# Optimization experiments

Measured on AMD Instinct MI355X. Metric: run time of the kernel, lower is better.

Reference implementation:

```python
import jax, jax.numpy as jnp
import numpy as np

N = 100001      # item_num + 1
D = 64          # hidden_units
NNZ = 3200000   # number of nonzeros in encoder_adj (avg degree ~32)


def setup_inputs() -> dict:
    key = jax.random.key(0)
    k1, k2, k3, k4 = jax.random.split(key, 4)
    row_idx = jax.random.randint(k1, (NNZ,), 0, N, dtype=jnp.int32)
    col_idx = jax.random.randint(k2, (NNZ,), 0, N, dtype=jnp.int32)
    adj_vals = jax.random.uniform(k3, (NNZ,), dtype=jnp.float32)
    emb_weight = jax.random.normal(k4, (N, D), dtype=jnp.float32)
    return {"row_idx": row_idx, "col_idx": col_idx, "adj_vals": adj_vals,
            "emb_weight": emb_weight}


def _spmm(row_idx, col_idx, vals, x):
    # COO SpMM: out[r] += vals[e] * x[col[e]]  -> [N, D]
    gathered = vals[:, None] * x[col_idx]          # [NNZ, D]
    return jax.ops.segment_sum(gathered, row_idx, num_segments=N)


def reference(row_idx, col_idx, adj_vals, emb_weight):
    e0 = emb_weight                                 # ego embeddings
    e1 = _spmm(row_idx, col_idx, adj_vals, e0)      # GCN layer 1
    e2 = _spmm(row_idx, col_idx, adj_vals, e1)      # GCN layer 2
    summed = e0 + e1 + e2                           # sum(embeds)
    return (summed, e0, e1, e2)
```

## Files before the change

kernel.cpp:

```cpp
#include <hip/hip_runtime.h>
#include <stdint.h>

#define DHID 64
#define G_BLOCKS 1024
#define BMAX 1024
#define RPB 128
#define CAP 4608

static inline size_t align256(size_t x) { return (x + 255) & ~(size_t)255; }


__global__ void zero_f32(float* __restrict__ p, size_t n) {
  size_t i = (size_t)blockIdx.x * blockDim.x + threadIdx.x;
  if (i < n) p[i] = 0.f;
}


__global__ __launch_bounds__(256) void
a1_hist_k(const int* __restrict__ row, int* __restrict__ histGB,
          int nnz, int B, int chunk) {
  __shared__ int h[BMAX];
  for (int i = threadIdx.x; i < B; i += 256) h[i] = 0;
  __syncthreads();
  int g = blockIdx.x;
  int s = g * chunk, e = min(nnz, s + chunk);
  int j = s + threadIdx.x;
  for (; j + 768 < e; j += 1024) {
    int r0 = row[j], r1 = row[j + 256], r2 = row[j + 512], r3 = row[j + 768];
    atomicAdd(&h[r0 >> 7], 1);
    atomicAdd(&h[r1 >> 7], 1);
    atomicAdd(&h[r2 >> 7], 1);
    atomicAdd(&h[r3 >> 7], 1);
  }
  for (; j < e; j += 256)
    atomicAdd(&h[row[j] >> 7], 1);
  __syncthreads();
  for (int i = threadIdx.x; i < B; i += 256)
    histGB[i * G_BLOCKS + g] = h[i];
}

__global__ __launch_bounds__(256) void
scan_gb_k(const int* __restrict__ histGB, int* __restrict__ offGB,
          int* __restrict__ btot, int B) {
  __shared__ int wsum[4];
  int b = blockIdx.x, t = threadIdx.x, lane = t & 63, w = t >> 6;
  int v[4];
  int s4 = 0;
#pragma unroll
  for (int i = 0; i < 4; ++i) {
    v[i] = histGB[b * G_BLOCKS + t * 4 + i];
    s4 += v[i];
  }
  int incl = s4;
#pragma unroll
  for (int off = 1; off < 64; off <<= 1) {
    int u = __shfl_up(incl, off);
    if (lane >= off) incl += u;
  }
  if (lane == 63) wsum[w] = incl;
  __syncthreads();
  int run = incl - s4;
  for (int w2 = 0; w2 < w; ++w2) run += wsum[w2];
#pragma unroll
  for (int i = 0; i < 4; ++i) {
    offGB[b * G_BLOCKS + t * 4 + i] = run;
    run += v[i];
  }
  if (t == 0) btot[b] = wsum[0] + wsum[1] + wsum[2] + wsum[3];
}

__global__ void scan_b_k(const int* __restrict__ btot, int* __restrict__ base, int B) {
  __shared__ int wsum[4];
  int t = threadIdx.x, lane = t & 63, w = t >> 6;
  int v[8];
  int s = 0;
#pragma unroll
  for (int i = 0; i < 8; ++i) {
    int idx = t * 8 + i;
    v[i] = (idx < B) ? btot[idx] : 0;
    s += v[i];
  }
  int incl = s;
#pragma unroll
  for (int off = 1; off < 64; off <<= 1) {
    int u = __shfl_up(incl, off);
    if (lane >= off) incl += u;
  }
  if (lane == 63) wsum[w] = incl;
  __syncthreads();
  int run = incl - s;
  for (int w2 = 0; w2 < w; ++w2) run += wsum[w2];
#pragma unroll
  for (int i = 0; i < 8; ++i) {
    int idx = t * 8 + i;
    if (idx <= B) base[idx] = run;
    run += v[i];
  }
}

__global__ __launch_bounds__(256) void
a2_scatter_k(const int* __restrict__ row, const int* __restrict__ col,
             const float* __restrict__ val, const int* __restrict__ base,
             const int* __restrict__ offGB, int2* __restrict__ stage,
             int nnz, int B, int chunk) {
  __shared__ int cur[BMAX];
  int g = blockIdx.x;
  for (int i = threadIdx.x; i < B; i += 256)
    cur[i] = base[i] + offGB[i * G_BLOCKS + g];
  __syncthreads();
  int s = g * chunk, e = min(nnz, s + chunk);
  int j = s + threadIdx.x;
  for (; j + 768 < e; j += 1024) {
    int r0 = row[j], r1 = row[j + 256], r2 = row[j + 512], r3 = row[j + 768];
    int c0 = col[j], c1 = col[j + 256], c2 = col[j + 512], c3 = col[j + 768];
    float v0 = val[j], v1 = val[j + 256], v2 = val[j + 512], v3 = val[j + 768];
    int p0 = atomicAdd(&cur[r0 >> 7], 1);
    int p1 = atomicAdd(&cur[r1 >> 7], 1);
    int p2 = atomicAdd(&cur[r2 >> 7], 1);
    int p3 = atomicAdd(&cur[r3 >> 7], 1);
    int2 q0; q0.x = ((r0 & 127) << 24) | c0; q0.y = __float_as_int(v0);
    int2 q1; q1.x = ((r1 & 127) << 24) | c1; q1.y = __float_as_int(v1);
    int2 q2; q2.x = ((r2 & 127) << 24) | c2; q2.y = __float_as_int(v2);
    int2 q3; q3.x = ((r3 & 127) << 24) | c3; q3.y = __float_as_int(v3);
    stage[p0] = q0;
    stage[p1] = q1;
    stage[p2] = q2;
    stage[p3] = q3;
  }
  for (; j < e; j += 256) {
    int r = row[j];
    int pos = atomicAdd(&cur[r >> 7], 1);
    int2 p;
    p.x = ((r & 127) << 24) | col[j];
    p.y = __float_as_int(val[j]);
    stage[pos] = p;
  }
}


__global__ __launch_bounds__(512) void
spmm_csr_k(const int* __restrict__ base, const int2* __restrict__ stage,
           const float* __restrict__ x, float* __restrict__ y, int n) {
  __shared__ int2 ebuf[CAP];
  __shared__ int h[RPB], rowoff[RPB], cur[RPB];
  __shared__ int w0sum;
  int b = blockIdx.x, t = threadIdx.x;
  int lane = t & 63, w = t >> 6;
  if (t < RPB) h[t] = 0;
  __syncthreads();
  int s = __builtin_amdgcn_readfirstlane(base[b]);
  int e = __builtin_amdgcn_readfirstlane(base[b + 1]);
  int cnt = e - s;
  if (cnt <= CAP) {
    for (int j = s + t; j < e; j += 512)
      atomicAdd(&h[((unsigned)stage[j].x) >> 24], 1);
    __syncthreads();
    int v = 0, part = 0;
    if (t < RPB) {
      v = h[t];
      int incl = v;
#pragma unroll
      for (int off = 1; off < 64; off <<= 1) {
        int u = __shfl_up(incl, off);
        if (lane >= off) incl += u;
      }
      if (t == 63) w0sum = incl;
      part = incl - v;
    }
    __syncthreads();
    if (t < RPB) {
      int excl = part + ((t >= 64) ? w0sum : 0);
      rowoff[t] = excl;
      cur[t] = excl;
    }
    __syncthreads();
    for (int j = s + t; j < e; j += 512) {
      int2 p = stage[j];
      int r = ((unsigned)p.x) >> 24;
      int pos = atomicAdd(&cur[r], 1);
      int2 q; q.x = p.x & 0xFFFFFF; q.y = p.y;
      ebuf[pos] = q;
    }
    __syncthreads();
    for (int rr = w * 16; rr < w * 16 + 16; ++rr) {
      int R = (b << 7) + rr;
      if (R >= n) continue;
      int start = __builtin_amdgcn_readfirstlane(rowoff[rr]);
      int end   = __builtin_amdgcn_readfirstlane(cur[rr]);
      float acc = 0.f;
      int k = start;
      for (; k + 8 <= end; k += 8) {
        int2 e0 = ebuf[k + 0], e1 = ebuf[k + 1], e2 = ebuf[k + 2], e3 = ebuf[k + 3];
        int2 e4 = ebuf[k + 4], e5 = ebuf[k + 5], e6 = ebuf[k + 6], e7 = ebuf[k + 7];
        float x0 = x[((size_t)e0.x << 6) + lane];
        float x1 = x[((size_t)e1.x << 6) + lane];
        float x2 = x[((size_t)e2.x << 6) + lane];
        float x3 = x[((size_t)e3.x << 6) + lane];
        float x4 = x[((size_t)e4.x << 6) + lane];
        float x5 = x[((size_t)e5.x << 6) + lane];
        float x6 = x[((size_t)e6.x << 6) + lane];
        float x7 = x[((size_t)e7.x << 6) + lane];
        acc += __int_as_float(e0.y) * x0;
        acc += __int_as_float(e1.y) * x1;
        acc += __int_as_float(e2.y) * x2;
        acc += __int_as_float(e3.y) * x3;
        acc += __int_as_float(e4.y) * x4;
        acc += __int_as_float(e5.y) * x5;
        acc += __int_as_float(e6.y) * x6;
        acc += __int_as_float(e7.y) * x7;
      }
      for (; k < end; ++k) {
        int2 p = ebuf[k];
        acc += __int_as_float(p.y) * x[((size_t)p.x << 6) + lane];
      }
      y[((size_t)R << 6) + lane] = acc;
    }
  } else {
    for (int rr = w * 16; rr < w * 16 + 16; ++rr) {
      int R = (b << 7) + rr;
      if (R >= n) continue;
      float acc = 0.f;
      for (int j = s; j < e; ++j) {
        int2 p = stage[j];
        if ((int)(((unsigned)p.x) >> 24) == rr)
          acc += __int_as_float(p.y) * x[((size_t)(p.x & 0xFFFFFF) << 6) + lane];
      }
      y[((size_t)R << 6) + lane] = acc;
    }
  }
}

__global__ __launch_bounds__(512) void
spmm_csr_fused_k(const int* __restrict__ base, const int2* __restrict__ stage,
                 const float* __restrict__ e0g, const float* __restrict__ e1g,
                 float* __restrict__ e2g, float* __restrict__ summed,
                 float* __restrict__ e0out, int n) {
  __shared__ int2 ebuf[CAP];
  __shared__ int h[RPB], rowoff[RPB], cur[RPB];
  __shared__ int w0sum;
  int b = blockIdx.x, t = threadIdx.x;
  int lane = t & 63, w = t >> 6;
  if (t < RPB) h[t] = 0;
  __syncthreads();
  int s = __builtin_amdgcn_readfirstlane(base[b]);
  int e = __builtin_amdgcn_readfirstlane(base[b + 1]);
  int cnt = e - s;
  if (cnt <= CAP) {
    for (int j = s + t; j < e; j += 512)
      atomicAdd(&h[((unsigned)stage[j].x) >> 24], 1);
    __syncthreads();
    int v = 0, part = 0;
    if (t < RPB) {
      v = h[t];
      int incl = v;
#pragma unroll
      for (int off = 1; off < 64; off <<= 1) {
        int u = __shfl_up(incl, off);
        if (lane >= off) incl += u;
      }
      if (t == 63) w0sum = incl;
      part = incl - v;
    }
    __syncthreads();
    if (t < RPB) {
      int excl = part + ((t >= 64) ? w0sum : 0);
      rowoff[t] = excl;
      cur[t] = excl;
    }
    __syncthreads();
    for (int j = s + t; j < e; j += 512) {
      int2 p = stage[j];
      int r = ((unsigned)p.x) >> 24;
      int pos = atomicAdd(&cur[r], 1);
      int2 q; q.x = p.x & 0xFFFFFF; q.y = p.y;
      ebuf[pos] = q;
    }
    __syncthreads();
    for (int rr = w * 16; rr < w * 16 + 16; ++rr) {
      int R = (b << 7) + rr;
      if (R >= n) continue;
      int start = __builtin_amdgcn_readfirstlane(rowoff[rr]);
      int end   = __builtin_amdgcn_readfirstlane(cur[rr]);
      float acc = 0.f;
      int k = start;
      for (; k + 8 <= end; k += 8) {
        int2 ea = ebuf[k + 0], eb = ebuf[k + 1], ec = ebuf[k + 2], ed = ebuf[k + 3];
        int2 ee = ebuf[k + 4], ef = ebuf[k + 5], eg = ebuf[k + 6], eh = ebuf[k + 7];
        float x0 = e1g[((size_t)ea.x << 6) + lane];
        float x1 = e1g[((size_t)eb.x << 6) + lane];
        float x2 = e1g[((size_t)ec.x << 6) + lane];
        float x3 = e1g[((size_t)ed.x << 6) + lane];
        float x4 = e1g[((size_t)ee.x << 6) + lane];
        float x5 = e1g[((size_t)ef.x << 6) + lane];
        float x6 = e1g[((size_t)eg.x << 6) + lane];
        float x7 = e1g[((size_t)eh.x << 6) + lane];
        acc += __int_as_float(ea.y) * x0;
        acc += __int_as_float(eb.y) * x1;
        acc += __int_as_float(ec.y) * x2;
        acc += __int_as_float(ed.y) * x3;
        acc += __int_as_float(ee.y) * x4;
        acc += __int_as_float(ef.y) * x5;
        acc += __int_as_float(eg.y) * x6;
        acc += __int_as_float(eh.y) * x7;
      }
      for (; k < end; ++k) {
        int2 p = ebuf[k];
        acc += __int_as_float(p.y) * e1g[((size_t)p.x << 6) + lane];
      }
      size_t o = ((size_t)R << 6) + lane;
      float v0 = e0g[o];
      float v1 = e1g[o];
      e2g[o] = acc;
      summed[o] = v0 + v1 + acc;
      e0out[o] = v0;
    }
  } else {
    for (int rr = w * 16; rr < w * 16 + 16; ++rr) {
      int R = (b << 7) + rr;
      if (R >= n) continue;
      float acc = 0.f;
      for (int j = s; j < e; ++j) {
        int2 p = stage[j];
        if ((int)(((unsigned)p.x) >> 24) == rr)
          acc += __int_as_float(p.y) * e1g[((size_t)(p.x & 0xFFFFFF) << 6) + lane];
      }
      size_t o = ((size_t)R << 6) + lane;
      float v0 = e0g[o];
      float v1 = e1g[o];
      e2g[o] = acc;
      summed[o] = v0 + v1 + acc;
      e0out[o] = v0;
    }
  }
}


__global__ void spmm_atomic_k(const int* __restrict__ row, const int* __restrict__ col,
                              const float* __restrict__ val, const float* __restrict__ x,
                              float* __restrict__ y, int nnz) {
  int wave = (blockIdx.x * blockDim.x + threadIdx.x) >> 6;
  int lane = threadIdx.x & 63;
  if (wave >= nnz) return;
  int r = row[wave]; int c = col[wave]; float v = val[wave];
  atomicAdd(&y[(size_t)r * DHID + lane], v * x[(size_t)c * DHID + lane]);
}

__global__ void sum_k(const float4* __restrict__ e0, const float4* __restrict__ e1,
                      const float4* __restrict__ e2, float4* __restrict__ summed,
                      float4* __restrict__ e0out, int n4) {
  int i = blockIdx.x * blockDim.x + threadIdx.x;
  if (i < n4) {
    float4 a = e0[i], b = e1[i], c = e2[i];
    float4 s;
    s.x = a.x + b.x + c.x;
    s.y = a.y + b.y + c.y;
    s.z = a.z + b.z + c.z;
    s.w = a.w + b.w + c.w;
    summed[i] = s;
    e0out[i] = a;
  }
}

extern "C" void kernel_launch(void* const* d_in, const int* in_sizes, int n_in,
                              void* d_out, int out_size, void* d_ws, size_t ws_size,
                              hipStream_t stream) {
  const int*   row = (const int*)d_in[0];
  const int*   col = (const int*)d_in[1];
  const float* val = (const float*)d_in[2];
  const float* emb = (const float*)d_in[3];
  int nnz = in_sizes[0];
  int n   = in_sizes[3] / DHID;
  size_t ND = (size_t)n * DHID;

  float* out    = (float*)d_out;
  float* summed = out;
  float* e0o    = out + ND;
  float* e1     = out + 2 * ND;
  float* e2     = out + 3 * ND;

  int B  = (n + RPB - 1) / RPB;
  int chunk = (nnz + G_BLOCKS - 1) / G_BLOCKS;

  size_t o0 = 0;
  size_t histGB_off = o0; o0 += align256((size_t)B * G_BLOCKS * 4);
  size_t offGB_off  = o0; o0 += align256((size_t)B * G_BLOCKS * 4);
  size_t btot_off   = o0; o0 += align256((size_t)B * 4);
  size_t base_off   = o0; o0 += align256((size_t)(B + 1) * 4);
  size_t stage_off  = o0; o0 += align256((size_t)nnz * 8);
  size_t need_sorted = o0;

  bool use_sorted = (ws_size >= need_sorted) && (B <= BMAX) && (n < (1 << 24));

  int n4 = (int)(ND / 4);
  int sb = (n4 + 255) / 256;
  int wb = (int)(((size_t)nnz * 64 + 255) / 256);

  if (use_sorted) {
    uint8_t* w = (uint8_t*)d_ws;
    int*  histGB = (int*)(w + histGB_off);
    int*  offGB  = (int*)(w + offGB_off);
    int*  btot   = (int*)(w + btot_off);
    int*  base   = (int*)(w + base_off);
    int2* stage  = (int2*)(w + stage_off);

    a1_hist_k<<<G_BLOCKS, 256, 0, stream>>>(row, histGB, nnz, B, chunk);
    scan_gb_k<<<B, 256, 0, stream>>>(histGB, offGB, btot, B);
    scan_b_k<<<1, 256, 0, stream>>>(btot, base, B);
    a2_scatter_k<<<G_BLOCKS, 256, 0, stream>>>(row, col, val, base, offGB, stage,
                                               nnz, B, chunk);

    spmm_csr_k<<<B, 512, 0, stream>>>(base, stage, emb, e1, n);
    spmm_csr_fused_k<<<B, 512, 0, stream>>>(base, stage, emb, e1, e2, summed, e0o, n);
  } else {
    zero_f32<<<(int)((ND + 255) / 256), 256, 0, stream>>>(e1, ND);
    spmm_atomic_k<<<wb, 256, 0, stream>>>(row, col, val, emb, e1, nnz);
    zero_f32<<<(int)((ND + 255) / 256), 256, 0, stream>>>(e2, ND);
    spmm_atomic_k<<<wb, 256, 0, stream>>>(row, col, val, e1, e2, nnz);
    sum_k<<<sb, 256, 0, stream>>>((const float4*)emb, (const float4*)e1,
                                  (const float4*)e2, (float4*)summed,
                                  (float4*)e0o, n4);
  }
}
```

Measured before the change: 432.6 us.

## Bucket edges by column phase so SpMM gathers sweep column ranges in lockstep

In both SpMM kernels, each block's edges are now bucketed by (column range of 16K rows, local row) rather than by local row alone. The gather loop then walks phase by phase, and all waves keep 16 row accumulators in registers. Within a phase every block reads from the same slice of x at roughly the same time, which is meant to improve L2/MALL hit rates for the random gathers. The cost is a scan over 1024 keys instead of 128, more LDS for the offset arrays, more registers, and a shorter unroll (4 instead of 8) for rows that are now split into smaller segments.

```diff
diff --git a/kernel.cpp b/kernel.cpp
--- a/kernel.cpp
+++ b/kernel.cpp
@@ -6,6 +6,9 @@
 #define BMAX 1024
 #define RPB 128
 #define CAP 4608
+#define PH_SHIFT 14
+#define NPHMAX 8
+#define NKEY (NPHMAX * RPB)
 
 static inline size_t align256(size_t x) { return (x + 255) & ~(size_t)255; }
 
@@ -140,80 +143,81 @@
 
 __global__ __launch_bounds__(512) void
 spmm_csr_k(const int* __restrict__ base, const int2* __restrict__ stage,
-           const float* __restrict__ x, float* __restrict__ y, int n) {
+           const float* __restrict__ x, float* __restrict__ y, int n, int nph) {
   __shared__ int2 ebuf[CAP];
-  __shared__ int h[RPB], rowoff[RPB], cur[RPB];
-  __shared__ int w0sum;
+  __shared__ int rowoff[NKEY], cur[NKEY];
+  __shared__ int wsum[8];
   int b = blockIdx.x, t = threadIdx.x;
   int lane = t & 63, w = t >> 6;
-  if (t < RPB) h[t] = 0;
+  cur[t] = 0; cur[t + 512] = 0;
   __syncthreads();
   int s = __builtin_amdgcn_readfirstlane(base[b]);
   int e = __builtin_amdgcn_readfirstlane(base[b + 1]);
   int cnt = e - s;
   if (cnt <= CAP) {
-    for (int j = s + t; j < e; j += 512)
-      atomicAdd(&h[((unsigned)stage[j].x) >> 24], 1);
-    __syncthreads();
-    int v = 0, part = 0;
-    if (t < RPB) {
-      v = h[t];
-      int incl = v;
-#pragma unroll
-      for (int off = 1; off < 64; off <<= 1) {
-        int u = __shfl_up(incl, off);
-        if (lane >= off) incl += u;
-      }
-      if (t == 63) w0sum = incl;
-      part = incl - v;
-    }
-    __syncthreads();
-    if (t < RPB) {
-      int excl = part + ((t >= 64) ? w0sum : 0);
-      rowoff[t] = excl;
-      cur[t] = excl;
-    }
-    __syncthreads();
     for (int j = s + t; j < e; j += 512) {
       int2 p = stage[j];
-      int r = ((unsigned)p.x) >> 24;
-      int pos = atomicAdd(&cur[r], 1);
+      int key = (((p.x & 0xFFFFFF) >> PH_SHIFT) << 7) | (((unsigned)p.x) >> 24);
+      atomicAdd(&cur[key], 1);
+    }
+    __syncthreads();
+    int v0 = cur[2 * t], v1 = cur[2 * t + 1];
+    int s2 = v0 + v1;
+    int incl = s2;
+#pragma unroll
+    for (int off = 1; off < 64; off <<= 1) {
+      int u = __shfl_up(incl, off);
+      if (lane >= off) incl += u;
+    }
+    if (lane == 63) wsum[w] = incl;
+    __syncthreads();
+    int run = incl - s2;
+    for (int w2 = 0; w2 < w; ++w2) run += wsum[w2];
+    rowoff[2 * t] = run;
+    rowoff[2 * t + 1] = run + v0;
+    cur[2 * t] = run;
+    cur[2 * t + 1] = run + v0;
+    __syncthreads();
+    for (int j = s + t; j < e; j += 512) {
+      int2 p = stage[j];
+      int key = (((p.x & 0xFFFFFF) >> PH_SHIFT) << 7) | (((unsigned)p.x) >> 24);
+      int pos = atomicAdd(&cur[key], 1);
       int2 q; q.x = p.x & 0xFFFFFF; q.y = p.y;
       ebuf[pos] = q;
     }
     __syncthreads();
-    for (int rr = w * 16; rr < w * 16 + 16; ++rr) {
-      int R = (b << 7) + rr;
-      if (R >= n) continue;
-      int start = __builtin_amdgcn_readfirstlane(rowoff[rr]);
-      int end   = __builtin_amdgcn_readfirstlane(cur[rr]);
-      float acc = 0.f;
-      int k = start;
-      for (; k + 8 <= end; k += 8) {
-        int2 e0 = ebuf[k + 0], e1 = ebuf[k + 1], e2 = ebuf[k + 2], e3 = ebuf[k + 3];
-        int2 e4 = ebuf[k + 4], e5 = ebuf[k + 5], e6 = ebuf[k + 6], e7 = ebuf[k + 7];
-        float x0 = x[((size_t)e0.x << 6) + lane];
-        float x1 = x[((size_t)e1.x << 6) + lane];
-        float x2 = x[((size_t)e2.x << 6) + lane];
-        float x3 = x[((size_t)e3.x << 6) + lane];
-        float x4 = x[((size_t)e4.x << 6) + lane];
-        float x5 = x[((size_t)e5.x << 6) + lane];
-        float x6 = x[((size_t)e6.x << 6) + lane];
-        float x7 = x[((size_t)e7.x << 6) + lane];
-        acc += __int_as_float(e0.y) * x0;
-        acc += __int_as_float(e1.y) * x1;
-        acc += __int_as_float(e2.y) * x2;
-        acc += __int_as_float(e3.y) * x3;
-        acc += __int_as_float(e4.y) * x4;
-        acc += __int_as_float(e5.y) * x5;
-        acc += __int_as_float(e6.y) * x6;
-        acc += __int_as_float(e7.y) * x7;
+    float acc[16];
+#pragma unroll
+    for (int i = 0; i < 16; ++i) acc[i] = 0.f;
+    for (int p = 0; p < nph; ++p) {
+#pragma unroll
+      for (int i = 0; i < 16; ++i) {
+        int key = (p << 7) | (w * 16 + i);
+        int k   = __builtin_amdgcn_readfirstlane(rowoff[key]);
+        int end = __builtin_amdgcn_readfirstlane(cur[key]);
+        float a = acc[i];
+        for (; k + 4 <= end; k += 4) {
+          int2 q0 = ebuf[k], q1 = ebuf[k + 1], q2 = ebuf[k + 2], q3 = ebuf[k + 3];
+          float x0 = x[((size_t)q0.x << 6) + lane];
+          float x1 = x[((size_t)q1.x << 6) + lane];
+          float x2 = x[((size_t)q2.x << 6) + lane];
+          float x3 = x[((size_t)q3.x << 6) + lane];
+          a += __int_as_float(q0.y) * x0;
+          a += __int_as_float(q1.y) * x1;
+          a += __int_as_float(q2.y) * x2;
+          a += __int_as_float(q3.y) * x3;
+        }
+        for (; k < end; ++k) {
+          int2 q = ebuf[k];
+          a += __int_as_float(q.y) * x[((size_t)q.x << 6) + lane];
+        }
+        acc[i] = a;
       }
-      for (; k < end; ++k) {
-        int2 p = ebuf[k];
-        acc += __int_as_float(p.y) * x[((size_t)p.x << 6) + lane];
-      }
-      y[((size_t)R << 6) + lane] = acc;
+    }
+#pragma unroll
+    for (int i = 0; i < 16; ++i) {
+      int R = (b << 7) + w * 16 + i;
+      if (R < n) y[((size_t)R << 6) + lane] = acc[i];
     }
   } else {
     for (int rr = w * 16; rr < w * 16 + 16; ++rr) {
@@ -234,85 +238,88 @@
 spmm_csr_fused_k(const int* __restrict__ base, const int2* __restrict__ stage,
                  const float* __restrict__ e0g, const float* __restrict__ e1g,
                  float* __restrict__ e2g, float* __restrict__ summed,
-                 float* __restrict__ e0out, int n) {
+                 float* __restrict__ e0out, int n, int nph) {
   __shared__ int2 ebuf[CAP];
-  __shared__ int h[RPB], rowoff[RPB], cur[RPB];
-  __shared__ int w0sum;
+  __shared__ int rowoff[NKEY], cur[NKEY];
+  __shared__ int wsum[8];
   int b = blockIdx.x, t = threadIdx.x;
   int lane = t & 63, w = t >> 6;
-  if (t < RPB) h[t] = 0;
+  cur[t] = 0; cur[t + 512] = 0;
   __syncthreads();
   int s = __builtin_amdgcn_readfirstlane(base[b]);
   int e = __builtin_amdgcn_readfirstlane(base[b + 1]);
   int cnt = e - s;
   if (cnt <= CAP) {
-    for (int j = s + t; j < e; j += 512)
-      atomicAdd(&h[((unsigned)stage[j].x) >> 24], 1);
-    __syncthreads();
-    int v = 0, part = 0;
-    if (t < RPB) {
-      v = h[t];
-      int incl = v;
-#pragma unroll
-      for (int off = 1; off < 64; off <<= 1) {
-        int u = __shfl_up(incl, off);
-        if (lane >= off) incl += u;
-      }
-      if (t == 63) w0sum = incl;
-      part = incl - v;
-    }
-    __syncthreads();
-    if (t < RPB) {
-      int excl = part + ((t >= 64) ? w0sum : 0);
-      rowoff[t] = excl;
-      cur[t] = excl;
-    }
-    __syncthreads();
     for (int j = s + t; j < e; j += 512) {
       int2 p = stage[j];
-      int r = ((unsigned)p.x) >> 24;
-      int pos = atomicAdd(&cur[r], 1);
+      int key = (((p.x & 0xFFFFFF) >> PH_SHIFT) << 7) | (((unsigned)p.x) >> 24);
+      atomicAdd(&cur[key], 1);
+    }
+    __syncthreads();
+    int v0 = cur[2 * t], v1 = cur[2 * t + 1];
+    int s2 = v0 + v1;
+    int incl = s2;
+#pragma unroll
+    for (int off = 1; off < 64; off <<= 1) {
+      int u = __shfl_up(incl, off);
+      if (lane >= off) incl += u;
+    }
+    if (lane == 63) wsum[w] = incl;
+    __syncthreads();
+    int run = incl - s2;
+    for (int w2 = 0; w2 < w; ++w2) run += wsum[w2];
+    rowoff[2 * t] = run;
+    rowoff[2 * t + 1] = run + v0;
+    cur[2 * t] = run;
+    cur[2 * t + 1] = run + v0;
+    __syncthreads();
+    for (int j = s + t; j < e; j += 512) {
+      int2 p = stage[j];
+      int key = (((p.x & 0xFFFFFF) >> PH_SHIFT) << 7) | (((unsigned)p.x) >> 24);
+      int pos = atomicAdd(&cur[key], 1);
       int2 q; q.x = p.x & 0xFFFFFF; q.y = p.y;
       ebuf[pos] = q;
     }
     __syncthreads();
-    for (int rr = w * 16; rr < w * 16 + 16; ++rr) {
-      int R = (b << 7) + rr;
-      if (R >= n) continue;
-      int start = __builtin_amdgcn_readfirstlane(rowoff[rr]);
-      int end   = __builtin_amdgcn_readfirstlane(cur[rr]);
-      float acc = 0.f;
-      int k = start;
-      for (; k + 8 <= end; k += 8) {
-        int2 ea = ebuf[k + 0], eb = ebuf[k + 1], ec = ebuf[k + 2], ed = ebuf[k + 3];
-        int2 ee = ebuf[k + 4], ef = ebuf[k + 5], eg = ebuf[k + 6], eh = ebuf[k + 7];
-        float x0 = e1g[((size_t)ea.x << 6) + lane];
-        float x1 = e1g[((size_t)eb.x << 6) + lane];
-        float x2 = e1g[((size_t)ec.x << 6) + lane];
-        float x3 = e1g[((size_t)ed.x << 6) + lane];
-        float x4 = e1g[((size_t)ee.x << 6) + lane];
-        float x5 = e1g[((size_t)ef.x << 6) + lane];
-        float x6 = e1g[((size_t)eg.x << 6) + lane];
-        float x7 = e1g[((size_t)eh.x << 6) + lane];
-        acc += __int_as_float(ea.y) * x0;
-        acc += __int_as_float(eb.y) * x1;
-        acc += __int_as_float(ec.y) * x2;
-        acc += __int_as_float(ed.y) * x3;
-        acc += __int_as_float(ee.y) * x4;
-        acc += __int_as_float(ef.y) * x5;
-        acc += __int_as_float(eg.y) * x6;
-        acc += __int_as_float(eh.y) * x7;
+    float acc[16];
+#pragma unroll
+    for (int i = 0; i < 16; ++i) acc[i] = 0.f;
+    for (int p = 0; p < nph; ++p) {
+#pragma unroll
+      for (int i = 0; i < 16; ++i) {
+        int key = (p << 7) | (w * 16 + i);
+        int k   = __builtin_amdgcn_readfirstlane(rowoff[key]);
+        int end = __builtin_amdgcn_readfirstlane(cur[key]);
+        float a = acc[i];
+        for (; k + 4 <= end; k += 4) {
+          int2 q0 = ebuf[k], q1 = ebuf[k + 1], q2 = ebuf[k + 2], q3 = ebuf[k + 3];
+          float x0 = e1g[((size_t)q0.x << 6) + lane];
+          float x1 = e1g[((size_t)q1.x << 6) + lane];
+          float x2 = e1g[((size_t)q2.x << 6) + lane];
+          float x3 = e1g[((size_t)q3.x << 6) + lane];
+          a += __int_as_float(q0.y) * x0;
+          a += __int_as_float(q1.y) * x1;
+          a += __int_as_float(q2.y) * x2;
+          a += __int_as_float(q3.y) * x3;
+        }
+        for (; k < end; ++k) {
+          int2 q = ebuf[k];
+          a += __int_as_float(q.y) * e1g[((size_t)q.x << 6) + lane];
+        }
+        acc[i] = a;
       }
-      for (; k < end; ++k) {
-        int2 p = ebuf[k];
-        acc += __int_as_float(p.y) * e1g[((size_t)p.x << 6) + lane];
+    }
+#pragma unroll
+    for (int i = 0; i < 16; ++i) {
+      int R = (b << 7) + w * 16 + i;
+      if (R < n) {
+        size_t o = ((size_t)R << 6) + lane;
+        float v0f = e0g[o];
+        float v1f = e1g[o];
+        e2g[o] = acc[i];
+        summed[o] = v0f + v1f + acc[i];
+        e0out[o] = v0f;
       }
-      size_t o = ((size_t)R << 6) + lane;
-      float v0 = e0g[o];
-      float v1 = e1g[o];
-      e2g[o] = acc;
-      summed[o] = v0 + v1 + acc;
-      e0out[o] = v0;
     }
   } else {
     for (int rr = w * 16; rr < w * 16 + 16; ++rr) {
@@ -379,6 +386,7 @@
   float* e2     = out + 3 * ND;
 
   int B  = (n + RPB - 1) / RPB;
+  int nph = (n + (1 << PH_SHIFT) - 1) >> PH_SHIFT;
   int chunk = (nnz + G_BLOCKS - 1) / G_BLOCKS;
 
   size_t o0 = 0;
@@ -389,7 +397,8 @@
   size_t stage_off  = o0; o0 += align256((size_t)nnz * 8);
   size_t need_sorted = o0;
 
-  bool use_sorted = (ws_size >= need_sorted) && (B <= BMAX) && (n < (1 << 24));
+  bool use_sorted = (ws_size >= need_sorted) && (B <= BMAX) && (n < (1 << 24)) &&
+                    (nph <= NPHMAX);
 
   int n4 = (int)(ND / 4);
   int sb = (n4 + 255) / 256;
@@ -409,8 +418,9 @@
     a2_scatter_k<<<G_BLOCKS, 256, 0, stream>>>(row, col, val, base, offGB, stage,
                                                nnz, B, chunk);
 
-    spmm_csr_k<<<B, 512, 0, stream>>>(base, stage, emb, e1, n);
-    spmm_csr_fused_k<<<B, 512, 0, stream>>>(base, stage, emb, e1, e2, summed, e0o, n);
+    spmm_csr_k<<<B, 512, 0, stream>>>(base, stage, emb, e1, n, nph);
+    spmm_csr_fused_k<<<B, 512, 0, stream>>>(base, stage, emb, e1, e2, summed, e0o,
+                                            n, nph);
   } else {
     zero_f32<<<(int)((ND + 255) / 256), 256, 0, stream>>>(e1, ND);
     spmm_atomic_k<<<wb, 256, 0, stream>>>(row, col, val, emb, e1, nnz);
```

New measurement: 589.2 us. +36.2%, slower.
